# Performance work log

Measured on AMD Instinct MI355X. Metric: run time of the kernel, lower is better.

Reference implementation:

```python
import jax, jax.numpy as jnp
import numpy as np

B, S, D_IN, D_MODEL, H = 4, 2048, 1024, 1024, 16
HD = D_MODEL // H  # head_dim = 64


def setup_inputs() -> dict:
    key = jax.random.key(0)
    ks = jax.random.split(key, 9)
    scale = 1.0 / np.sqrt(D_IN)
    return {
        "Q": jax.random.normal(ks[0], (B, S, D_IN), jnp.float32),
        "V": jax.random.normal(ks[1], (B, S, D_IN), jnp.float32),
        "K": jax.random.normal(ks[2], (B, S, D_IN), jnp.float32),
        "wq": jax.random.uniform(ks[3], (D_IN, D_MODEL), jnp.float32, -scale, scale),
        "bq": jax.random.uniform(ks[4], (D_MODEL,), jnp.float32, -scale, scale),
        "wk": jax.random.uniform(ks[5], (D_IN, D_MODEL), jnp.float32, -scale, scale),
        "bk": jax.random.uniform(ks[6], (D_MODEL,), jnp.float32, -scale, scale),
        "wv": jax.random.uniform(ks[7], (D_IN, D_MODEL), jnp.float32, -scale, scale),
        "bv": jax.random.uniform(ks[8], (D_MODEL,), jnp.float32, -scale, scale),
    }


def _split_heads(x):
    # [B,S,D] -> [B,H,S,HD]
    return x.reshape(B, S, H, HD).transpose(0, 2, 1, 3)


def reference(Q, V, K, wq, bq, wk, bk, wv, bv):
    q = _split_heads(Q @ wq + bq)
    k = _split_heads(K @ wk + bk)
    v = _split_heads(V @ wv + bv)
    scores = jnp.einsum("bhqd,bhkd->bhqk", q, k) / jnp.sqrt(jnp.float32(HD))
    weights = jax.nn.softmax(scores, axis=-1)
    out = jnp.einsum("bhqk,bhkd->bhqd", weights, v)
    return out.transpose(0, 2, 1, 3).reshape(B, S, D_MODEL)
```

## Files before the change

kernel.cpp:

```cpp
#include <hip/hip_runtime.h>
#include <hip/hip_bf16.h>

typedef unsigned short u16;
typedef __attribute__((ext_vector_type(8))) short bf16x8;
typedef __attribute__((ext_vector_type(4))) float f32x4;
typedef __attribute__((ext_vector_type(4))) unsigned short u16x4;
typedef __attribute__((ext_vector_type(2))) unsigned u32x2;

#define NB 4
#define NS 2048
#define DIN 1024
#define DM 1024
#define NH 16
#define HD 64
#define LOG2E 1.44269504f

__device__ __forceinline__ u16 f2bf(float f) {
  union { float f; unsigned u; } x; x.f = f;
  unsigned r = x.u + 0x7fffu + ((x.u >> 16) & 1u);
  return (u16)(r >> 16);
}

__device__ __forceinline__ unsigned pk_bf16(float a, float b) {
  union { __hip_bfloat162 h; unsigned u; } cv;
  cv.h = __float22bfloat162_rn(make_float2(a, b));
  return cv.u;
}

__device__ __forceinline__ void gl_lds16(const u16* g, u16* l) {
  __builtin_amdgcn_global_load_lds((const __attribute__((address_space(1))) void*)g,
                                   (__attribute__((address_space(3))) void*)l, 16, 0, 0);
}

__global__ void prep_kernel(const float* __restrict__ Qp, const float* __restrict__ Kp,
                            const float* __restrict__ Vp, u16* __restrict__ oq,
                            u16* __restrict__ ok, u16* __restrict__ ov,
                            const float* __restrict__ wqp, const float* __restrict__ wkp,
                            const float* __restrict__ wvp, u16* __restrict__ owq,
                            u16* __restrict__ owk, u16* __restrict__ owv, int n4) {
  __shared__ float tile[64][65];
  const int b = blockIdx.x, t = threadIdx.x;
  if (b < 3072) {
    const int ten = b >> 10, bx = b & 1023;
    const float* s = ten == 0 ? Qp : ten == 1 ? Kp : Vp;
    u16* d = ten == 0 ? oq : ten == 1 ? ok : ov;
    int stride = 1024 * 256;
    for (int i = bx * 256 + t; i < n4; i += stride) {
      f32x4 v = ((const f32x4*)s)[i];
      u32x2 o;
      o.x = pk_bf16(v.x, v.y);
      o.y = pk_bf16(v.z, v.w);
      ((u32x2*)d)[i] = o;
    }
  } else {
    const int wt = b - 3072;
    const int z = wt >> 8, rem = wt & 255;
    const float* W = z == 0 ? wqp : z == 1 ? wkp : wvp;
    u16* Wt = z == 0 ? owq : z == 1 ? owk : owv;
    int n0 = (rem & 15) * 64, k0 = (rem >> 4) * 64;
#pragma unroll
    for (int i = 0; i < 16; i++) {
      int idx = t + i * 256;
      int r = idx >> 6, c = idx & 63;
      tile[r][c] = W[(size_t)(k0 + r) * DM + n0 + c];
    }
    __syncthreads();
#pragma unroll
    for (int i = 0; i < 16; i++) {
      int idx = t + i * 256;
      int r = idx >> 6, c = idx & 63;
      Wt[(size_t)(n0 + r) * DIN + k0 + c] = f2bf(tile[c][r]);
    }
  }
}

__global__ __launch_bounds__(256) void proj_kernel(
    const u16* __restrict__ Xq, const u16* __restrict__ Xk, const u16* __restrict__ Xv,
    const u16* __restrict__ Wtq, const u16* __restrict__ Wtk, const u16* __restrict__ Wtv,
    const float* __restrict__ bq, const float* __restrict__ bk, const float* __restrict__ bv,
    u16* __restrict__ oq, u16* __restrict__ ok, u16* __restrict__ ov) {
  __shared__ __align__(16) u16 Abuf[128 * 64];
  __shared__ __align__(16) u16 Bbuf[128 * 64];
  const int bid = blockIdx.x;
  const int xr = bid & 7;
  const int nt = (bid >> 3) & 7;
  const int mt = (bid >> 6) & 7;
  const int z  = bid >> 9;
  const int m0 = (mt * 8 + xr) * 128, n0 = nt * 128;
  const u16* X  = z == 0 ? Xq : z == 1 ? Xk : Xv;
  const u16* Wt = z == 0 ? Wtq : z == 1 ? Wtk : Wtv;
  const float* bias = z == 0 ? bq : z == 1 ? bk : bv;
  u16* out = z == 0 ? oq : z == 1 ? ok : ov;
  const int t = threadIdx.x, lane = t & 63, w = t >> 6;
  const int c = lane & 15, g = lane >> 4;
  const int wm = (w >> 1) * 64, wn = (w & 1) * 64;
  f32x4 acc[4][4] = {};
  for (int k0 = 0; k0 < DIN; k0 += 64) {
#pragma unroll
    for (int i = 0; i < 4; i++) {
      int idx = (w * 4 + i) * 64 + lane;
      int row = idx >> 3;
      int srck = (idx & 7) ^ (row & 7);
      gl_lds16(&X [(size_t)(m0 + row) * DIN + k0 + srck * 8], &Abuf[(w * 4 + i) * 512]);
      gl_lds16(&Wt[(size_t)(n0 + row) * DIN + k0 + srck * 8], &Bbuf[(w * 4 + i) * 512]);
    }
    __syncthreads();
#pragma unroll
    for (int ks = 0; ks < 2; ks++) {
      bf16x8 xf[4], wf[4];
      int chn = ((ks * 4 + g) ^ (c & 7)) * 8;
#pragma unroll
      for (int a = 0; a < 4; a++) {
        xf[a] = *(const bf16x8*)&Abuf[(wm + a * 16 + c) * 64 + chn];
        wf[a] = *(const bf16x8*)&Bbuf[(wn + a * 16 + c) * 64 + chn];
      }
      if (z < 2) {
#pragma unroll
        for (int i = 0; i < 4; i++)
#pragma unroll
          for (int j = 0; j < 4; j++)
            acc[i][j] = __builtin_amdgcn_mfma_f32_16x16x32_bf16(wf[i], xf[j], acc[i][j], 0, 0, 0);
      } else {
#pragma unroll
        for (int i = 0; i < 4; i++)
#pragma unroll
          for (int j = 0; j < 4; j++)
            acc[i][j] = __builtin_amdgcn_mfma_f32_16x16x32_bf16(xf[i], wf[j], acc[i][j], 0, 0, 0);
      }
    }
    __syncthreads();
  }
  if (z < 2) {
    const float sc = (z == 0) ? 0.125f * LOG2E : 1.0f;
#pragma unroll
    for (int i = 0; i < 4; i++) {
      int nb = n0 + wn + i * 16 + g * 4;
      int h = nb >> 6, d0 = nb & 63;
      f32x4 bv4 = *(const f32x4*)&bias[nb];
#pragma unroll
      for (int j = 0; j < 4; j++) {
        int mm = m0 + wm + j * 16 + c;
        int b = mm >> 11, s = mm & 2047;
        u16x4 pk;
#pragma unroll
        for (int r = 0; r < 4; r++) pk[r] = f2bf((acc[i][j][r] + bv4[r]) * sc);
        *(u16x4*)&out[((size_t)(b * NH + h) * NS + s) * HD + d0] = pk;
      }
    }
  } else {
#pragma unroll
    for (int j = 0; j < 4; j++) {
      int n = n0 + wn + j * 16 + c;
      int h = n >> 6, d = n & 63;
      float bvs = bias[n];
#pragma unroll
      for (int i = 0; i < 4; i++) {
        int mb = m0 + wm + i * 16 + g * 4;
        int b = mb >> 11, s0 = mb & 2047;
        u16x4 pk;
#pragma unroll
        for (int r = 0; r < 4; r++) pk[r] = f2bf(acc[i][j][r] + bvs);
        *(u16x4*)&out[((size_t)(b * NH + h) * HD + d) * NS + s0] = pk;
      }
    }
  }
}

#define NG 2
__global__ __launch_bounds__(256, 2) void attn_kernel(
    const u16* __restrict__ q, const u16* __restrict__ k, const u16* __restrict__ vT,
    float* __restrict__ out) {
  __shared__ __align__(16) u16 kt[64 * 64];
  __shared__ __align__(16) u16 vt[64 * 64];
  __shared__ __align__(16) u16 pt_all[4][NG * 16 * 64];
  const int bid = blockIdx.x;
  const int xr = bid & 7;
  const int qc = (bid >> 3) & 15;
  const int h8 = bid >> 7;
  const int bh = xr + 8 * h8;
  const int t = threadIdx.x, lane = t & 63, w = t >> 6;
  const int c = lane & 15, g = lane >> 4;
  const int q0 = qc * 128 + w * 32;
  u16* pt = pt_all[w];
  const u16* qsrc = q + ((size_t)bh * NS + q0) * HD;
  const u16* ksrc = k + (size_t)bh * NS * HD;
  const u16* vsrc = vT + (size_t)bh * HD * NS;
  const int srow = lane >> 3;
  const int skc = (lane & 7) ^ srow;
  bf16x8 qf[NG][2];
#pragma unroll
  for (int grp = 0; grp < NG; grp++)
#pragma unroll
    for (int ks = 0; ks < 2; ks++)
      qf[grp][ks] = *(const bf16x8*)&qsrc[(grp * 16 + c) * HD + ks * 32 + g * 8];
  bf16x8 ones;
#pragma unroll
  for (int i = 0; i < 8; i++) ones[i] = (short)0x3F80;
  f32x4 o[NG][4] = {};
  f32x4 ol[NG] = {};
  for (int kt0 = 0; kt0 < NS; kt0 += 64) {
#pragma unroll
    for (int j = 0; j < 2; j++) {
      int row = w * 16 + j * 8 + srow;
      gl_lds16(&ksrc[(size_t)(kt0 + row) * HD + skc * 8], &kt[(w * 16 + j * 8) * 64]);
      gl_lds16(&vsrc[(size_t)row * NS + kt0 + skc * 8], &vt[(w * 16 + j * 8) * 64]);
    }
    __syncthreads();
    bf16x8 kf[4][2];
#pragma unroll
    for (int kg = 0; kg < 4; kg++)
#pragma unroll
      for (int ks = 0; ks < 2; ks++)
        kf[kg][ks] = *(const bf16x8*)&kt[(kg * 16 + c) * 64 + (((ks * 4 + g) ^ (c & 7)) * 8)];
#pragma unroll
    for (int grp = 0; grp < NG; grp++) {
      f32x4 s4[4] = {};
      __builtin_amdgcn_s_setprio(1);
#pragma unroll
      for (int ks = 0; ks < 2; ks++)
#pragma unroll
        for (int kg = 0; kg < 4; kg++)
          s4[kg] = __builtin_amdgcn_mfma_f32_16x16x32_bf16(kf[kg][ks], qf[grp][ks], s4[kg], 0, 0, 0);
      __builtin_amdgcn_s_setprio(0);
#pragma unroll
      for (int kg = 0; kg < 4; kg++) {
        u32x2 pk;
        pk.x = pk_bf16(__builtin_amdgcn_exp2f(s4[kg][0]), __builtin_amdgcn_exp2f(s4[kg][1]));
        pk.y = pk_bf16(__builtin_amdgcn_exp2f(s4[kg][2]), __builtin_amdgcn_exp2f(s4[kg][3]));
        *(u32x2*)&pt[(grp * 16 + c) * 64 + (((kg * 2 + (g >> 1)) ^ (c & 7)) * 8) + (g & 1) * 4] = pk;
      }
    }
#pragma unroll
    for (int ks = 0; ks < 2; ks++) {
      bf16x8 vf4[4];
#pragma unroll
      for (int dj = 0; dj < 4; dj++)
        vf4[dj] = *(const bf16x8*)&vt[(dj * 16 + c) * 64 + (((ks * 4 + g) ^ (c & 7)) * 8)];
#pragma unroll
      for (int grp = 0; grp < NG; grp++) {
        bf16x8 pf = *(const bf16x8*)&pt[(grp * 16 + c) * 64 + (((ks * 4 + g) ^ (c & 7)) * 8)];
        __builtin_amdgcn_s_setprio(1);
#pragma unroll
        for (int dj = 0; dj < 4; dj++)
          o[grp][dj] = __builtin_amdgcn_mfma_f32_16x16x32_bf16(vf4[dj], pf, o[grp][dj], 0, 0, 0);
        ol[grp] = __builtin_amdgcn_mfma_f32_16x16x32_bf16(ones, pf, ol[grp], 0, 0, 0);
        __builtin_amdgcn_s_setprio(0);
      }
    }
    __syncthreads();
  }
  const int b = bh >> 4, h = bh & 15;
#pragma unroll
  for (int grp = 0; grp < NG; grp++) {
    float inv = 1.f / ol[grp][0];
    int s = q0 + grp * 16 + c;
#pragma unroll
    for (int dj = 0; dj < 4; dj++) {
      f32x4 ov = o[grp][dj] * inv;
      *(f32x4*)&out[((size_t)b * NS + s) * DM + h * HD + dj * 16 + g * 4] = ov;
    }
  }
}

extern "C" void kernel_launch(void* const* d_in, const int* in_sizes, int n_in,
                              void* d_out, int out_size, void* d_ws, size_t ws_size,
                              hipStream_t stream) {
  const float* Q  = (const float*)d_in[0];
  const float* V  = (const float*)d_in[1];
  const float* K  = (const float*)d_in[2];
  const float* wq = (const float*)d_in[3];
  const float* bq = (const float*)d_in[4];
  const float* wk = (const float*)d_in[5];
  const float* bk = (const float*)d_in[6];
  const float* wv = (const float*)d_in[7];
  const float* bv = (const float*)d_in[8];
  float* out = (float*)d_out;
  char* ws = (char*)d_ws;
  const size_t NX = (size_t)NB * NS * DIN;
  const size_t XB = NX * 2;
  const size_t WB = (size_t)DIN * DM * 2;
  u16* Xq   = (u16*)(ws);
  u16* Xk   = (u16*)(ws + XB);
  u16* Xv   = (u16*)(ws + 2 * XB);
  u16* Wtq  = (u16*)(ws + 3 * XB);
  u16* Wtk  = (u16*)(ws + 3 * XB + WB);
  u16* Wtv  = (u16*)(ws + 3 * XB + 2 * WB);
  u16* qws  = (u16*)(ws + 3 * XB + 3 * WB);
  u16* kws  = (u16*)(ws + 4 * XB + 3 * WB);
  u16* vTws = (u16*)(ws + 5 * XB + 3 * WB);
  const int n4 = (int)(NX / 4);
  prep_kernel<<<3840, 256, 0, stream>>>(Q, K, V, Xq, Xk, Xv,
                                        wq, wk, wv, Wtq, Wtk, Wtv, n4);
  proj_kernel<<<1536, 256, 0, stream>>>(Xq, Xk, Xv, Wtq, Wtk, Wtv,
                                        bq, bk, bv, qws, kws, vTws);
  attn_kernel<<<1024, 256, 0, stream>>>(qws, kws, vTws, out);
}
```

Measured before the change: 309.7 us.

## Switch attention to 32x32x16 MFMA and pass P through lanes instead of LDS

Rewrites the attention inner loop to use 32x32x16 bf16 MFMA tiles instead of 16x16x32. The exp'd score tile is packed to bf16 and rearranged into the PV operand layout with permlane32_swap, which removes the per-wave LDS round trip for the probability matrix. The row-sum is now computed with scalar adds plus one cross-half shuffle rather than an extra MFMA against a ones vector. This cuts LDS traffic and MFMA count, but changes register pressure and the accumulator layout.

```diff
diff --git a/kernel.cpp b/kernel.cpp
--- a/kernel.cpp
+++ b/kernel.cpp
@@ -4,6 +4,7 @@
 typedef unsigned short u16;
 typedef __attribute__((ext_vector_type(8))) short bf16x8;
 typedef __attribute__((ext_vector_type(4))) float f32x4;
+typedef __attribute__((ext_vector_type(16))) float f32x16;
 typedef __attribute__((ext_vector_type(4))) unsigned short u16x4;
 typedef __attribute__((ext_vector_type(2))) unsigned u32x2;
 
@@ -166,38 +167,30 @@
   }
 }
 
-#define NG 2
 __global__ __launch_bounds__(256, 2) void attn_kernel(
     const u16* __restrict__ q, const u16* __restrict__ k, const u16* __restrict__ vT,
     float* __restrict__ out) {
   __shared__ __align__(16) u16 kt[64 * 64];
   __shared__ __align__(16) u16 vt[64 * 64];
-  __shared__ __align__(16) u16 pt_all[4][NG * 16 * 64];
   const int bid = blockIdx.x;
   const int xr = bid & 7;
   const int qc = (bid >> 3) & 15;
   const int h8 = bid >> 7;
   const int bh = xr + 8 * h8;
   const int t = threadIdx.x, lane = t & 63, w = t >> 6;
-  const int c = lane & 15, g = lane >> 4;
+  const int h = lane >> 5, ql = lane & 31, c7 = lane & 7;
   const int q0 = qc * 128 + w * 32;
-  u16* pt = pt_all[w];
   const u16* qsrc = q + ((size_t)bh * NS + q0) * HD;
   const u16* ksrc = k + (size_t)bh * NS * HD;
   const u16* vsrc = vT + (size_t)bh * HD * NS;
   const int srow = lane >> 3;
   const int skc = (lane & 7) ^ srow;
-  bf16x8 qf[NG][2];
-#pragma unroll
-  for (int grp = 0; grp < NG; grp++)
-#pragma unroll
-    for (int ks = 0; ks < 2; ks++)
-      qf[grp][ks] = *(const bf16x8*)&qsrc[(grp * 16 + c) * HD + ks * 32 + g * 8];
-  bf16x8 ones;
-#pragma unroll
-  for (int i = 0; i < 8; i++) ones[i] = (short)0x3F80;
-  f32x4 o[NG][4] = {};
-  f32x4 ol[NG] = {};
+  bf16x8 qf[4];
+#pragma unroll
+  for (int ks = 0; ks < 4; ks++)
+    qf[ks] = *(const bf16x8*)&qsrc[ql * HD + ks * 16 + h * 8];
+  f32x16 o32[2] = {};
+  float lacc = 0.f;
   for (int kt0 = 0; kt0 < NS; kt0 += 64) {
 #pragma unroll
     for (int j = 0; j < 2; j++) {
@@ -206,60 +199,61 @@
       gl_lds16(&vsrc[(size_t)row * NS + kt0 + skc * 8], &vt[(w * 16 + j * 8) * 64]);
     }
     __syncthreads();
-    bf16x8 kf[4][2];
-#pragma unroll
-    for (int kg = 0; kg < 4; kg++)
-#pragma unroll
-      for (int ks = 0; ks < 2; ks++)
-        kf[kg][ks] = *(const bf16x8*)&kt[(kg * 16 + c) * 64 + (((ks * 4 + g) ^ (c & 7)) * 8)];
-#pragma unroll
-    for (int grp = 0; grp < NG; grp++) {
-      f32x4 s4[4] = {};
+#pragma unroll
+    for (int kb = 0; kb < 2; kb++) {
+      f32x16 s32 = {};
       __builtin_amdgcn_s_setprio(1);
 #pragma unroll
-      for (int ks = 0; ks < 2; ks++)
-#pragma unroll
-        for (int kg = 0; kg < 4; kg++)
-          s4[kg] = __builtin_amdgcn_mfma_f32_16x16x32_bf16(kf[kg][ks], qf[grp][ks], s4[kg], 0, 0, 0);
+      for (int ks = 0; ks < 4; ks++) {
+        bf16x8 ka = *(const bf16x8*)&kt[(kb * 32 + ql) * 64 + (((ks * 2 + h) ^ c7) * 8)];
+        s32 = __builtin_amdgcn_mfma_f32_32x32x16_bf16(ka, qf[ks], s32, 0, 0, 0);
+      }
       __builtin_amdgcn_s_setprio(0);
-#pragma unroll
-      for (int kg = 0; kg < 4; kg++) {
-        u32x2 pk;
-        pk.x = pk_bf16(__builtin_amdgcn_exp2f(s4[kg][0]), __builtin_amdgcn_exp2f(s4[kg][1]));
-        pk.y = pk_bf16(__builtin_amdgcn_exp2f(s4[kg][2]), __builtin_amdgcn_exp2f(s4[kg][3]));
-        *(u32x2*)&pt[(grp * 16 + c) * 64 + (((kg * 2 + (g >> 1)) ^ (c & 7)) * 8) + (g & 1) * 4] = pk;
-      }
-    }
-#pragma unroll
-    for (int ks = 0; ks < 2; ks++) {
-      bf16x8 vf4[4];
-#pragma unroll
-      for (int dj = 0; dj < 4; dj++)
-        vf4[dj] = *(const bf16x8*)&vt[(dj * 16 + c) * 64 + (((ks * 4 + g) ^ (c & 7)) * 8)];
-#pragma unroll
-      for (int grp = 0; grp < NG; grp++) {
-        bf16x8 pf = *(const bf16x8*)&pt[(grp * 16 + c) * 64 + (((ks * 4 + g) ^ (c & 7)) * 8)];
+      float e[16];
+#pragma unroll
+      for (int r = 0; r < 16; r++) e[r] = __builtin_amdgcn_exp2f(s32[r]);
+      {
+        float t0 = (e[0] + e[1]) + (e[2] + e[3]);
+        float t1 = (e[4] + e[5]) + (e[6] + e[7]);
+        float t2 = (e[8] + e[9]) + (e[10] + e[11]);
+        float t3 = (e[12] + e[13]) + (e[14] + e[15]);
+        lacc += (t0 + t1) + (t2 + t3);
+      }
+#pragma unroll
+      for (int s = 0; s < 2; s++) {
+        unsigned A  = pk_bf16(e[8 * s + 0], e[8 * s + 1]);
+        unsigned Bp = pk_bf16(e[8 * s + 2], e[8 * s + 3]);
+        unsigned C  = pk_bf16(e[8 * s + 4], e[8 * s + 5]);
+        unsigned D  = pk_bf16(e[8 * s + 6], e[8 * s + 7]);
+        u32x2 r02 = __builtin_amdgcn_permlane32_swap(A, C, false, false);
+        u32x2 r13 = __builtin_amdgcn_permlane32_swap(Bp, D, false, false);
+        union { unsigned u[4]; bf16x8 v; } pf;
+        pf.u[0] = r02.x; pf.u[1] = r13.x; pf.u[2] = r02.y; pf.u[3] = r13.y;
+        const int ksl = kb * 2 + s;
         __builtin_amdgcn_s_setprio(1);
 #pragma unroll
-        for (int dj = 0; dj < 4; dj++)
-          o[grp][dj] = __builtin_amdgcn_mfma_f32_16x16x32_bf16(vf4[dj], pf, o[grp][dj], 0, 0, 0);
-        ol[grp] = __builtin_amdgcn_mfma_f32_16x16x32_bf16(ones, pf, ol[grp], 0, 0, 0);
+        for (int db = 0; db < 2; db++) {
+          bf16x8 va = *(const bf16x8*)&vt[(db * 32 + ql) * 64 + (((ksl * 2 + h) ^ c7) * 8)];
+          o32[db] = __builtin_amdgcn_mfma_f32_32x32x16_bf16(va, pf.v, o32[db], 0, 0, 0);
+        }
         __builtin_amdgcn_s_setprio(0);
       }
     }
     __syncthreads();
   }
-  const int b = bh >> 4, h = bh & 15;
-#pragma unroll
-  for (int grp = 0; grp < NG; grp++) {
-    float inv = 1.f / ol[grp][0];
-    int s = q0 + grp * 16 + c;
-#pragma unroll
-    for (int dj = 0; dj < 4; dj++) {
-      f32x4 ov = o[grp][dj] * inv;
-      *(f32x4*)&out[((size_t)b * NS + s) * DM + h * HD + dj * 16 + g * 4] = ov;
-    }
-  }
+  const float lq = lacc + __shfl_xor(lacc, 32);
+  const float inv = 1.f / lq;
+  const int b = bh >> 4, hh = bh & 15;
+  const int s_idx = q0 + ql;
+  float* obase = &out[((size_t)b * NS + s_idx) * DM + hh * HD];
+#pragma unroll
+  for (int db = 0; db < 2; db++)
+#pragma unroll
+    for (int i = 0; i < 4; i++) {
+      f32x4 ov = { o32[db][4 * i + 0] * inv, o32[db][4 * i + 1] * inv,
+                   o32[db][4 * i + 2] * inv, o32[db][4 * i + 3] * inv };
+      *(f32x4*)&obase[db * 32 + 8 * i + 4 * h] = ov;
+    }
 }
 
 extern "C" void kernel_launch(void* const* d_in, const int* in_sizes, int n_in,
```

Result: no change. 304.4 us (median of 3 runs) (-1.7%).
